# Kernel optimization log

Hardware: AMD Instinct MI355X
Metric: run time of the kernel (lower is better)

The kernel has to match this reference:

```python
import jax, jax.numpy as jnp
import numpy as np

IN_FEAT = 3 * 32 * 32  # channels*height*width
HID = 1024
CLASSES = 10
EPS = 1e-5


def binarize(w):
    # Deterministic BinaryConnect: sign(w) in {-1, +1} (sign(0) -> +1)
    return jnp.where(w >= 0, 1.0, -1.0).astype(w.dtype)


def batchnorm(h, gamma, beta):
    # training-mode BatchNorm1d: biased batch stats over batch axis
    mean = jnp.mean(h, axis=0)
    var = jnp.var(h, axis=0)
    return gamma * (h - mean) * jax.lax.rsqrt(var + EPS) + beta


def setup_inputs() -> dict:
    key = jax.random.key(0)
    ks = jax.random.split(key, 6)
    x = jax.random.normal(ks[0], (8192, 3, 32, 32), dtype=jnp.float32)
    # latent real-valued weights, torch Linear layout [out, in], kaiming-ish scale
    W1 = jax.random.normal(ks[1], (HID, IN_FEAT), dtype=jnp.float32) * (1.0 / np.sqrt(IN_FEAT))
    W2 = jax.random.normal(ks[2], (HID, HID), dtype=jnp.float32) * (1.0 / np.sqrt(HID))
    W3 = jax.random.normal(ks[3], (HID, HID), dtype=jnp.float32) * (1.0 / np.sqrt(HID))
    W4 = jax.random.normal(ks[4], (CLASSES, HID), dtype=jnp.float32) * (1.0 / np.sqrt(HID))
    g1 = jnp.ones((HID,), jnp.float32); b1 = jnp.zeros((HID,), jnp.float32)
    g2 = jnp.ones((HID,), jnp.float32); b2 = jnp.zeros((HID,), jnp.float32)
    g3 = jnp.ones((HID,), jnp.float32); b3 = jnp.zeros((HID,), jnp.float32)
    return {"x": x, "W1": W1, "W2": W2, "W3": W3, "W4": W4,
            "g1": g1, "b1": b1, "g2": g2, "b2": b2, "g3": g3, "b3": b3}


def reference(x, W1, W2, W3, W4, g1, b1, g2, b2, g3, b3):
    h = x.reshape(-1, IN_FEAT)                       # [B, 3072]
    h = jax.nn.relu(h @ binarize(W1).T)              # [B, 1024]
    h = batchnorm(h, g1, b1)
    h = jax.nn.relu(h @ binarize(W2).T)
    h = batchnorm(h, g2, b2)
    h = jax.nn.relu(h @ binarize(W3).T)
    h = batchnorm(h, g3, b3)
    return h @ binarize(W4).T                        # [B, classes]
```

## Files before the change

kernel.cpp:

```cpp
#include <hip/hip_runtime.h>
#include <stdint.h>

typedef unsigned short u16;
typedef __attribute__((ext_vector_type(8))) unsigned short ushort8;
typedef __attribute__((ext_vector_type(4))) unsigned short ushort4v;
typedef __attribute__((ext_vector_type(8))) __bf16 bf16x8;
typedef __attribute__((ext_vector_type(4))) __bf16 bf16x4;
typedef __attribute__((ext_vector_type(4))) float f32x4;

__device__ __forceinline__ u16 f2bf(float f) {
    union { float f; unsigned int u; } v; v.f = f;
    unsigned int r = v.u + 0x7FFFu + ((v.u >> 16) & 1u);
    return (u16)(r >> 16);
}
__device__ __forceinline__ float bf2f(u16 b) {
    union { unsigned int u; float f; } v; v.u = ((unsigned int)b) << 16;
    return v.f;
}

typedef __attribute__((address_space(1))) const uint32_t* gptr_t;
typedef __attribute__((address_space(3))) uint32_t* lptr_t;
__device__ __forceinline__ void async_copy16(const void* g, void* l) {
    __builtin_amdgcn_global_load_lds((gptr_t)g, (lptr_t)l, 16, 0, 0);
}


__global__ __launch_bounds__(256) void binarize_kernel(
    const float* __restrict__ in, u16* __restrict__ out, int n8)
{
    int i = blockIdx.x * 256 + threadIdx.x;
    if (i >= n8) return;
    const float4* p = (const float4*)(in + (size_t)i * 8);
    float4 x0 = p[0], x1 = p[1];
    ushort8 o;
    o[0] = x0.x >= 0.f ? 0x3F80 : 0xBF80;
    o[1] = x0.y >= 0.f ? 0x3F80 : 0xBF80;
    o[2] = x0.z >= 0.f ? 0x3F80 : 0xBF80;
    o[3] = x0.w >= 0.f ? 0x3F80 : 0xBF80;
    o[4] = x1.x >= 0.f ? 0x3F80 : 0xBF80;
    o[5] = x1.y >= 0.f ? 0x3F80 : 0xBF80;
    o[6] = x1.z >= 0.f ? 0x3F80 : 0xBF80;
    o[7] = x1.w >= 0.f ? 0x3F80 : 0xBF80;
    *(ushort8*)(out + (size_t)i * 8) = o;
}

__global__ __launch_bounds__(256) void build_w4t(
    const float* __restrict__ W4, u16* __restrict__ W4T)
{
    int idx = blockIdx.x * 256 + threadIdx.x;
    int k = idx >> 4, c = idx & 15;
    u16 v = 0;
    if (c < 10) v = (W4[(size_t)c * 1024 + k] >= 0.f) ? 0x3F80 : 0xBF80;
    W4T[idx] = v;
}

__global__ __launch_bounds__(256) void rescale_w(
    const float* __restrict__ W, const float* __restrict__ ss,
    u16* __restrict__ Wp, float* __restrict__ bias)
{
    const int lane = threadIdx.x & 63;
    const int wid  = threadIdx.x >> 6;
    const int r    = blockIdx.x * 4 + wid;
    float bsum = 0.f;
    #pragma unroll
    for (int k0 = 0; k0 < 1024; k0 += 256) {
        int k = k0 + lane * 4;
        float4 w  = *(const float4*)(W + (size_t)r * 1024 + k);
        float4 sc = *(const float4*)(ss + k);
        float4 sh = *(const float4*)(ss + 1024 + k);
        ushort4v o;
        o[0] = f2bf(w.x >= 0.f ? sc.x : -sc.x);
        o[1] = f2bf(w.y >= 0.f ? sc.y : -sc.y);
        o[2] = f2bf(w.z >= 0.f ? sc.z : -sc.z);
        o[3] = f2bf(w.w >= 0.f ? sc.w : -sc.w);
        bsum += (w.x >= 0.f ? sh.x : -sh.x) + (w.y >= 0.f ? sh.y : -sh.y)
              + (w.z >= 0.f ? sh.z : -sh.z) + (w.w >= 0.f ? sh.w : -sh.w);
        *(ushort4v*)(Wp + (size_t)r * 1024 + k) = o;
    }
    #pragma unroll
    for (int off = 32; off; off >>= 1) bsum += __shfl_xor(bsum, off, 64);
    if (lane == 0) bias[r] = bsum;
}


__global__ __launch_bounds__(256) void gemm1_f32a(
    const float* __restrict__ A, const u16* __restrict__ B,
    u16* __restrict__ H,
    float* __restrict__ partS, float* __restrict__ partS2,
    int M, int N, int K)
{
    __shared__ __align__(16) u16 As[2][128 * 64];
    __shared__ __align__(16) u16 Bs[2][128 * 64];

    const int tid  = threadIdx.x;
    const int wid  = tid >> 6;
    const int lane = tid & 63;
    const int lr   = lane & 15;
    const int hk   = lane >> 4;
    const int x7   = lr & 7;
    const int wr   = wid >> 1;
    const int wc   = wid & 1;
    const int row0 = blockIdx.x * 128;
    const int col0 = blockIdx.y * 128;

    const int s_r = tid >> 3;
    const int s_c = (((tid & 7) ^ (s_r & 7)) << 3);
    const u16* gB = B + (size_t)(col0 + s_r) * K + s_c;

    const int a_r = tid >> 4;
    const int a_c = (tid & 15) * 4;
    const float* gA = A + (size_t)(row0 + a_r) * K + a_c;
    const int a_c8 = (tid & 15) >> 1;
    const int a_cw = (tid & 1) * 4;
    float4 areg[8];

    int a_base[4], b_base[4];
    #pragma unroll
    for (int i = 0; i < 4; ++i) a_base[i] = (wr * 64 + i * 16 + lr) * 64;
    #pragma unroll
    for (int j = 0; j < 4; ++j) b_base[j] = (wc * 64 + j * 16 + lr) * 64;
    const int xs0 = ((hk)     ^ x7) << 3;
    const int xs1 = ((hk + 4) ^ x7) << 3;

    f32x4 acc[4][4];
    #pragma unroll
    for (int i = 0; i < 4; ++i)
        #pragma unroll
        for (int j = 0; j < 4; ++j)
            acc[i][j] = (f32x4){0.f, 0.f, 0.f, 0.f};

    const int NT = K >> 6;

    auto LOADA = [&](int t) {
        const float* p = gA + (size_t)t * 64;
        #pragma unroll
        for (int i = 0; i < 8; ++i)
            areg[i] = *(const float4*)(p + (size_t)i * 16 * K);
    };
    auto WRITEA = [&](int buf) {
        #pragma unroll
        for (int i = 0; i < 8; ++i) {
            int row = i * 16 + a_r;
            u16* dst = &As[buf][row * 64 + ((a_c8 ^ (row & 7)) << 3) + a_cw];
            bf16x4 o = { (__bf16)areg[i].x, (__bf16)areg[i].y,
                         (__bf16)areg[i].z, (__bf16)areg[i].w };
            *(bf16x4*)dst = o;
        }
    };
    auto STAGEB = [&](int buf, int t) {
        const u16* pb = gB + (size_t)t * 64;
        #pragma unroll
        for (int i = 0; i < 4; ++i)
            async_copy16(pb + (size_t)i * 32 * K, &Bs[buf][i * 2048 + wid * 512]);
    };

    LOADA(0);
    WRITEA(0);
    LOADA(1);
    STAGEB(0, 0);
    WRITEA(1);
    LOADA(2);
    STAGEB(1, 1);
    asm volatile("s_waitcnt lgkmcnt(0)" ::: "memory");

    for (int t = 0; t < NT; ++t) {
        const int buf = t & 1;
        if (t + 1 < NT) asm volatile("s_waitcnt vmcnt(12)" ::: "memory");
        else            asm volatile("s_waitcnt vmcnt(0)" ::: "memory");
        __builtin_amdgcn_s_barrier();

        bf16x8 af[4][2], bg[4][2];
        #pragma unroll
        for (int i = 0; i < 4; ++i) {
            af[i][0] = *(const bf16x8*)&As[buf][a_base[i] + xs0];
            af[i][1] = *(const bf16x8*)&As[buf][a_base[i] + xs1];
        }
        #pragma unroll
        for (int j = 0; j < 4; ++j) {
            bg[j][0] = *(const bf16x8*)&Bs[buf][b_base[j] + xs0];
            bg[j][1] = *(const bf16x8*)&Bs[buf][b_base[j] + xs1];
        }
        asm volatile("s_waitcnt lgkmcnt(0)" ::: "memory");
        __builtin_amdgcn_sched_barrier(0);
        __builtin_amdgcn_s_barrier();

        WRITEA(buf);
        const int ta = (t + 3 < NT) ? t + 3 : NT - 1;
        LOADA(ta);
        const int tb = (t + 2 < NT) ? t + 2 : NT - 1;
        STAGEB(buf, tb);

        __builtin_amdgcn_s_setprio(1);
        #pragma unroll
        for (int kk = 0; kk < 2; ++kk)
            #pragma unroll
            for (int i = 0; i < 4; ++i)
                #pragma unroll
                for (int j = 0; j < 4; ++j)
                    acc[i][j] = __builtin_amdgcn_mfma_f32_16x16x32_bf16(
                        af[i][kk], bg[j][kk], acc[i][j], 0, 0, 0);
        __builtin_amdgcn_s_setprio(0);
    }

    const int er = hk * 4;
    #pragma unroll
    for (int j = 0; j < 4; ++j) {
        const int c = col0 + wc * 64 + j * 16 + lr;
        float s = 0.f, s2 = 0.f;
        #pragma unroll
        for (int i = 0; i < 4; ++i) {
            const int r = row0 + wr * 64 + i * 16 + er;
            #pragma unroll
            for (int b2 = 0; b2 < 4; ++b2) {
                float x = acc[i][j][b2];
                x = x > 0.f ? x : 0.f;
                s += x; s2 += x * x;
                H[(size_t)(r + b2) * N + c] = f2bf(x);
            }
        }
        s  += __shfl_xor(s, 16, 64);  s  += __shfl_xor(s, 32, 64);
        s2 += __shfl_xor(s2, 16, 64); s2 += __shfl_xor(s2, 32, 64);
        if (hk == 0) {
            const int p = blockIdx.x * 2 + wr;
            partS [(size_t)p * 1024 + c] = s;
            partS2[(size_t)p * 1024 + c] = s2;
        }
    }
}


__global__ __launch_bounds__(256) void gemm_fused(
    const u16* __restrict__ A, const u16* __restrict__ B,
    u16* __restrict__ H, const float* __restrict__ bias,
    float* __restrict__ partS, float* __restrict__ partS2,
    int M, int N, int K)
{
    __shared__ __align__(16) u16 As[2][128 * 64];
    __shared__ __align__(16) u16 Bs[2][128 * 64];

    const int tid  = threadIdx.x;
    const int wid  = tid >> 6;
    const int lane = tid & 63;
    const int lr   = lane & 15;
    const int hk   = lane >> 4;
    const int x7   = lr & 7;
    const int wr   = wid >> 1;
    const int wc   = wid & 1;
    const int row0 = blockIdx.x * 128;
    const int col0 = blockIdx.y * 128;

    const int s_r = tid >> 3;
    const int s_c = (((tid & 7) ^ (s_r & 7)) << 3);
    const u16* gA = A + (size_t)(row0 + s_r) * K + s_c;
    const u16* gB = B + (size_t)(col0 + s_r) * K + s_c;

    int a_base[4], b_base[4];
    #pragma unroll
    for (int i = 0; i < 4; ++i) a_base[i] = (wr * 64 + i * 16 + lr) * 64;
    #pragma unroll
    for (int j = 0; j < 4; ++j) b_base[j] = (wc * 64 + j * 16 + lr) * 64;
    const int xs0 = ((hk)     ^ x7) << 3;
    const int xs1 = ((hk + 4) ^ x7) << 3;

    f32x4 acc[4][4];
    #pragma unroll
    for (int i = 0; i < 4; ++i)
        #pragma unroll
        for (int j = 0; j < 4; ++j)
            acc[i][j] = (f32x4){0.f, 0.f, 0.f, 0.f};

    const int NT = K >> 6;

    auto STAGE = [&](int buf, int t) {
        const u16* pa = gA + (size_t)t * 64;
        const u16* pb = gB + (size_t)t * 64;
        #pragma unroll
        for (int i = 0; i < 4; ++i)
            async_copy16(pa + (size_t)i * 32 * K, &As[buf][i * 2048 + wid * 512]);
        #pragma unroll
        for (int i = 0; i < 4; ++i)
            async_copy16(pb + (size_t)i * 32 * K, &Bs[buf][i * 2048 + wid * 512]);
    };

    STAGE(0, 0);
    STAGE(1, 1);

    for (int t = 0; t < NT; ++t) {
        const int buf = t & 1;
        if (t + 1 < NT) asm volatile("s_waitcnt vmcnt(8)" ::: "memory");
        else            asm volatile("s_waitcnt vmcnt(0)" ::: "memory");
        __builtin_amdgcn_s_barrier();

        bf16x8 af[4][2], bg[4][2];
        #pragma unroll
        for (int i = 0; i < 4; ++i) {
            af[i][0] = *(const bf16x8*)&As[buf][a_base[i] + xs0];
            af[i][1] = *(const bf16x8*)&As[buf][a_base[i] + xs1];
        }
        #pragma unroll
        for (int j = 0; j < 4; ++j) {
            bg[j][0] = *(const bf16x8*)&Bs[buf][b_base[j] + xs0];
            bg[j][1] = *(const bf16x8*)&Bs[buf][b_base[j] + xs1];
        }
        asm volatile("s_waitcnt lgkmcnt(0)" ::: "memory");
        __builtin_amdgcn_sched_barrier(0);
        __builtin_amdgcn_s_barrier();

        if (t + 2 < NT) STAGE(buf, t + 2);

        __builtin_amdgcn_s_setprio(1);
        #pragma unroll
        for (int kk = 0; kk < 2; ++kk)
            #pragma unroll
            for (int i = 0; i < 4; ++i)
                #pragma unroll
                for (int j = 0; j < 4; ++j)
                    acc[i][j] = __builtin_amdgcn_mfma_f32_16x16x32_bf16(
                        af[i][kk], bg[j][kk], acc[i][j], 0, 0, 0);
        __builtin_amdgcn_s_setprio(0);
    }

    const int er = hk * 4;
    #pragma unroll
    for (int j = 0; j < 4; ++j) {
        const int c = col0 + wc * 64 + j * 16 + lr;
        const float bj = bias[c];
        float s = 0.f, s2 = 0.f;
        #pragma unroll
        for (int i = 0; i < 4; ++i) {
            const int r = row0 + wr * 64 + i * 16 + er;
            #pragma unroll
            for (int b2 = 0; b2 < 4; ++b2) {
                float x = acc[i][j][b2] + bj;
                x = x > 0.f ? x : 0.f;
                s += x; s2 += x * x;
                H[(size_t)(r + b2) * N + c] = f2bf(x);
            }
        }
        s  += __shfl_xor(s, 16, 64);  s  += __shfl_xor(s, 32, 64);
        s2 += __shfl_xor(s2, 16, 64); s2 += __shfl_xor(s2, 32, 64);
        if (hk == 0) {
            const int p = blockIdx.x * 2 + wr;
            partS [(size_t)p * 1024 + c] = s;
            partS2[(size_t)p * 1024 + c] = s2;
        }
    }
}


__global__ __launch_bounds__(256) void bn_finalize(
    const float* __restrict__ partS, const float* __restrict__ partS2,
    const float* __restrict__ gamma, const float* __restrict__ beta,
    float* __restrict__ ss)
{
    int c = blockIdx.x * 256 + threadIdx.x;
    float s = 0.f, s2 = 0.f;
    for (int i = 0; i < 128; ++i) {
        s  += partS [(size_t)i * 1024 + c];
        s2 += partS2[(size_t)i * 1024 + c];
    }
    float mean = s * (1.0f / 8192.0f);
    float var  = fmaxf(s2 * (1.0f / 8192.0f) - mean * mean, 0.f);
    float sc   = gamma[c] * rsqrtf(var + 1e-5f);
    ss[c]        = sc;
    ss[1024 + c] = beta[c] - mean * sc;
}


__global__ __launch_bounds__(256) void head_kernel(
    const u16* __restrict__ H, const u16* __restrict__ W4T,
    const float* __restrict__ ss, float* __restrict__ out)
{
    const int lane = threadIdx.x & 63;
    const int wid  = threadIdx.x >> 6;
    const int r    = blockIdx.x * 4 + wid;

    float acc[10];
    #pragma unroll
    for (int c = 0; c < 10; c++) acc[c] = 0.f;

    #pragma unroll
    for (int j = 0; j < 16; ++j) {
        int k = j * 64 + lane;
        float a = fmaf(bf2f(H[(size_t)r * 1024 + k]), ss[k], ss[1024 + k]);
        ushort8 w0 = *(const ushort8*)(W4T + (size_t)k * 16);
        acc[0] += a * bf2f(w0[0]); acc[1] += a * bf2f(w0[1]);
        acc[2] += a * bf2f(w0[2]); acc[3] += a * bf2f(w0[3]);
        acc[4] += a * bf2f(w0[4]); acc[5] += a * bf2f(w0[5]);
        acc[6] += a * bf2f(w0[6]); acc[7] += a * bf2f(w0[7]);
        u16 w8 = W4T[(size_t)k * 16 + 8];
        u16 w9 = W4T[(size_t)k * 16 + 9];
        acc[8] += a * bf2f(w8);    acc[9] += a * bf2f(w9);
    }
    #pragma unroll
    for (int c = 0; c < 10; c++) {
        float s = acc[c];
        #pragma unroll
        for (int off = 32; off > 0; off >>= 1) s += __shfl_xor(s, off, 64);
        acc[c] = s;
    }
    if (lane == 0) {
        #pragma unroll
        for (int c = 0; c < 10; c++) out[(size_t)r * 10 + c] = acc[c];
    }
}


extern "C" void kernel_launch(void* const* d_in, const int* in_sizes, int n_in,
                              void* d_out, int out_size, void* d_ws, size_t ws_size,
                              hipStream_t stream) {
    const float* x  = (const float*)d_in[0];
    const float* W1 = (const float*)d_in[1];
    const float* W2 = (const float*)d_in[2];
    const float* W3 = (const float*)d_in[3];
    const float* W4 = (const float*)d_in[4];
    const float* g1 = (const float*)d_in[5];
    const float* b1 = (const float*)d_in[6];
    const float* g2 = (const float*)d_in[7];
    const float* b2 = (const float*)d_in[8];
    const float* g3 = (const float*)d_in[9];
    const float* b3 = (const float*)d_in[10];
    float* out = (float*)d_out;

    char* ws = (char*)d_ws;
    u16*   Hb0    = (u16*)  (ws + 0);
    u16*   Hb1    = (u16*)  (ws + 16777216);
    u16*   W1b    = (u16*)  (ws + 33554432);
    u16*   W2p    = (u16*)  (ws + 39845888);
    u16*   W3p    = (u16*)  (ws + 41943040);
    u16*   W4T    = (u16*)  (ws + 44040192);
    float* partS  = (float*)(ws + 44072960);
    float* partS2 = (float*)(ws + 44597248);
    float* ss     = (float*)(ws + 45121536);
    float* bias2  = (float*)(ws + 45129728);
    float* bias3  = (float*)(ws + 45133824);

    binarize_kernel<<<1536, 256, 0, stream>>>(W1, W1b, 393216);
    build_w4t<<<64, 256, 0, stream>>>(W4, W4T);

    dim3 gemm_grid(64, 8);

    gemm1_f32a<<<gemm_grid, 256, 0, stream>>>(x, W1b, Hb0, partS, partS2, 8192, 1024, 3072);
    bn_finalize<<<4, 256, 0, stream>>>(partS, partS2, g1, b1, ss);
    rescale_w<<<256, 256, 0, stream>>>(W2, ss, W2p, bias2);

    gemm_fused<<<gemm_grid, 256, 0, stream>>>(Hb0, W2p, Hb1, bias2, partS, partS2, 8192, 1024, 1024);
    bn_finalize<<<4, 256, 0, stream>>>(partS, partS2, g2, b2, ss);
    rescale_w<<<256, 256, 0, stream>>>(W3, ss, W3p, bias3);

    gemm_fused<<<gemm_grid, 256, 0, stream>>>(Hb1, W3p, Hb0, bias3, partS, partS2, 8192, 1024, 1024);
    bn_finalize<<<4, 256, 0, stream>>>(partS, partS2, g3, b3, ss);

    head_kernel<<<2048, 256, 0, stream>>>(Hb0, W4T, ss, out);
}
```

Measured before the change: 197.1 us.

## Remap GEMM blocks across XCDs and deepen fp32 A prefetch in layer-1 GEMM

Adds an XCD-aware block index mapping so that blocks sharing the same A row tile are placed on the same chiplet, which should raise L2 reuse in both GEMM kernels. The layer-1 GEMM also keeps two register sets for the fp32 A tiles and unrolls the loop by two, prefetching A four tiles ahead instead of three. This hides more global-load latency for the large fp32 input at the cost of extra VGPRs and possible occupancy pressure. The mapping assumes an 8x8 column grid and a fixed grid shape.

```diff
diff --git a/kernel.cpp b/kernel.cpp
--- a/kernel.cpp
+++ b/kernel.cpp
@@ -82,6 +82,12 @@
     if (lane == 0) bias[r] = bsum;
 }
 
+__device__ __forceinline__ void xcd_map(int& mm, int& jj) {
+    const int d = blockIdx.x + blockIdx.y * gridDim.x;
+    mm = (d & 7) + (d >> 6) * 8;
+    jj = (d >> 3) & 7;
+}
+
 
 __global__ __launch_bounds__(256) void gemm1_f32a(
     const float* __restrict__ A, const u16* __restrict__ B,
@@ -100,8 +106,11 @@
     const int x7   = lr & 7;
     const int wr   = wid >> 1;
     const int wc   = wid & 1;
-    const int row0 = blockIdx.x * 128;
-    const int col0 = blockIdx.y * 128;
+
+    int mm, jj;
+    xcd_map(mm, jj);
+    const int row0 = mm * 128;
+    const int col0 = jj * 128;
 
     const int s_r = tid >> 3;
     const int s_c = (((tid & 7) ^ (s_r & 7)) << 3);
@@ -112,7 +121,7 @@
     const float* gA = A + (size_t)(row0 + a_r) * K + a_c;
     const int a_c8 = (tid & 15) >> 1;
     const int a_cw = (tid & 1) * 4;
-    float4 areg[8];
+    float4 aregA[8], aregB[8];
 
     int a_base[4], b_base[4];
     #pragma unroll
@@ -131,19 +140,35 @@
 
     const int NT = K >> 6;
 
-    auto LOADA = [&](int t) {
+    auto LOADA0 = [&](int t) {
         const float* p = gA + (size_t)t * 64;
         #pragma unroll
         for (int i = 0; i < 8; ++i)
-            areg[i] = *(const float4*)(p + (size_t)i * 16 * K);
-    };
-    auto WRITEA = [&](int buf) {
+            aregA[i] = *(const float4*)(p + (size_t)i * 16 * K);
+    };
+    auto LOADA1 = [&](int t) {
+        const float* p = gA + (size_t)t * 64;
+        #pragma unroll
+        for (int i = 0; i < 8; ++i)
+            aregB[i] = *(const float4*)(p + (size_t)i * 16 * K);
+    };
+    auto WRITEA0 = [&](int buf) {
         #pragma unroll
         for (int i = 0; i < 8; ++i) {
             int row = i * 16 + a_r;
             u16* dst = &As[buf][row * 64 + ((a_c8 ^ (row & 7)) << 3) + a_cw];
-            bf16x4 o = { (__bf16)areg[i].x, (__bf16)areg[i].y,
-                         (__bf16)areg[i].z, (__bf16)areg[i].w };
+            bf16x4 o = { (__bf16)aregA[i].x, (__bf16)aregA[i].y,
+                         (__bf16)aregA[i].z, (__bf16)aregA[i].w };
+            *(bf16x4*)dst = o;
+        }
+    };
+    auto WRITEA1 = [&](int buf) {
+        #pragma unroll
+        for (int i = 0; i < 8; ++i) {
+            int row = i * 16 + a_r;
+            u16* dst = &As[buf][row * 64 + ((a_c8 ^ (row & 7)) << 3) + a_cw];
+            bf16x4 o = { (__bf16)aregB[i].x, (__bf16)aregB[i].y,
+                         (__bf16)aregB[i].z, (__bf16)aregB[i].w };
             *(bf16x4*)dst = o;
         }
     };
@@ -154,53 +179,56 @@
             async_copy16(pb + (size_t)i * 32 * K, &Bs[buf][i * 2048 + wid * 512]);
     };
 
-    LOADA(0);
-    WRITEA(0);
-    LOADA(1);
+    LOADA0(0);
+    LOADA1(1);
+    WRITEA0(0);
     STAGEB(0, 0);
-    WRITEA(1);
-    LOADA(2);
+    WRITEA1(1);
+    LOADA0(2);
     STAGEB(1, 1);
+    LOADA1(3);
     asm volatile("s_waitcnt lgkmcnt(0)" ::: "memory");
 
-    for (int t = 0; t < NT; ++t) {
-        const int buf = t & 1;
-        if (t + 1 < NT) asm volatile("s_waitcnt vmcnt(12)" ::: "memory");
-        else            asm volatile("s_waitcnt vmcnt(0)" ::: "memory");
-        __builtin_amdgcn_s_barrier();
-
-        bf16x8 af[4][2], bg[4][2];
-        #pragma unroll
-        for (int i = 0; i < 4; ++i) {
-            af[i][0] = *(const bf16x8*)&As[buf][a_base[i] + xs0];
-            af[i][1] = *(const bf16x8*)&As[buf][a_base[i] + xs1];
-        }
-        #pragma unroll
-        for (int j = 0; j < 4; ++j) {
-            bg[j][0] = *(const bf16x8*)&Bs[buf][b_base[j] + xs0];
-            bg[j][1] = *(const bf16x8*)&Bs[buf][b_base[j] + xs1];
-        }
-        asm volatile("s_waitcnt lgkmcnt(0)" ::: "memory");
-        __builtin_amdgcn_sched_barrier(0);
-        __builtin_amdgcn_s_barrier();
-
-        WRITEA(buf);
-        const int ta = (t + 3 < NT) ? t + 3 : NT - 1;
-        LOADA(ta);
-        const int tb = (t + 2 < NT) ? t + 2 : NT - 1;
-        STAGEB(buf, tb);
-
-        __builtin_amdgcn_s_setprio(1);
-        #pragma unroll
-        for (int kk = 0; kk < 2; ++kk)
-            #pragma unroll
-            for (int i = 0; i < 4; ++i)
-                #pragma unroll
-                for (int j = 0; j < 4; ++j)
-                    acc[i][j] = __builtin_amdgcn_mfma_f32_16x16x32_bf16(
-                        af[i][kk], bg[j][kk], acc[i][j], 0, 0, 0);
-        __builtin_amdgcn_s_setprio(0);
-    }
+#define G1_ITER(T, WRITEA_f, LOADA_f)                                        \
+    {                                                                        \
+        const int buf_ = (T) & 1;                                            \
+        if ((T) + 1 < NT) asm volatile("s_waitcnt vmcnt(12)" ::: "memory");  \
+        else              asm volatile("s_waitcnt vmcnt(0)"  ::: "memory");  \
+        __builtin_amdgcn_s_barrier();                                        \
+        bf16x8 af[4][2], bg[4][2];                                           \
+        _Pragma("unroll")                                                    \
+        for (int i = 0; i < 4; ++i) {                                        \
+            af[i][0] = *(const bf16x8*)&As[buf_][a_base[i] + xs0];           \
+            af[i][1] = *(const bf16x8*)&As[buf_][a_base[i] + xs1];           \
+        }                                                                    \
+        _Pragma("unroll")                                                    \
+        for (int j = 0; j < 4; ++j) {                                        \
+            bg[j][0] = *(const bf16x8*)&Bs[buf_][b_base[j] + xs0];           \
+            bg[j][1] = *(const bf16x8*)&Bs[buf_][b_base[j] + xs1];           \
+        }                                                                    \
+        asm volatile("s_waitcnt lgkmcnt(0)" ::: "memory");                   \
+        __builtin_amdgcn_sched_barrier(0);                                   \
+        __builtin_amdgcn_s_barrier();                                        \
+        STAGEB(buf_, ((T) + 2 < NT) ? (T) + 2 : NT - 1);                     \
+        WRITEA_f(buf_);                                                      \
+        LOADA_f(((T) + 4 < NT) ? (T) + 4 : NT - 1);                          \
+        __builtin_amdgcn_s_setprio(1);                                       \
+        _Pragma("unroll")                                                    \
+        for (int kk = 0; kk < 2; ++kk)                                       \
+            _Pragma("unroll")                                                \
+            for (int i = 0; i < 4; ++i)                                      \
+                _Pragma("unroll")                                            \
+                for (int j = 0; j < 4; ++j)                                  \
+                    acc[i][j] = __builtin_amdgcn_mfma_f32_16x16x32_bf16(     \
+                        af[i][kk], bg[j][kk], acc[i][j], 0, 0, 0);           \
+        __builtin_amdgcn_s_setprio(0);                                       \
+    }
+
+    for (int t = 0; t < NT; t += 2) {
+        G1_ITER(t,     WRITEA0, LOADA0);
+        G1_ITER(t + 1, WRITEA1, LOADA1);
+    }
+#undef G1_ITER
 
     const int er = hk * 4;
     #pragma unroll
@@ -221,7 +249,7 @@
         s  += __shfl_xor(s, 16, 64);  s  += __shfl_xor(s, 32, 64);
         s2 += __shfl_xor(s2, 16, 64); s2 += __shfl_xor(s2, 32, 64);
         if (hk == 0) {
-            const int p = blockIdx.x * 2 + wr;
+            const int p = mm * 2 + wr;
             partS [(size_t)p * 1024 + c] = s;
             partS2[(size_t)p * 1024 + c] = s2;
         }
@@ -246,8 +274,11 @@
     const int x7   = lr & 7;
     const int wr   = wid >> 1;
     const int wc   = wid & 1;
-    const int row0 = blockIdx.x * 128;
-    const int col0 = blockIdx.y * 128;
+
+    int mm, jj;
+    xcd_map(mm, jj);
+    const int row0 = mm * 128;
+    const int col0 = jj * 128;
 
     const int s_r = tid >> 3;
     const int s_c = (((tid & 7) ^ (s_r & 7)) << 3);
@@ -340,7 +371,7 @@
         s  += __shfl_xor(s, 16, 64);  s  += __shfl_xor(s, 32, 64);
         s2 += __shfl_xor(s2, 16, 64); s2 += __shfl_xor(s2, 32, 64);
         if (hk == 0) {
-            const int p = blockIdx.x * 2 + wr;
+            const int p = mm * 2 + wr;
             partS [(size_t)p * 1024 + c] = s;
             partS2[(size_t)p * 1024 + c] = s2;
         }
```

Measured after the change: 196.7 us. About the same (-0.2%).
